# Kernel optimization log

Hardware: AMD Instinct MI355X
Metric: run time of the kernel (lower is better)

The kernel has to match this reference:

```python
import jax, jax.numpy as jnp
import numpy as np

V, L, H, D, DFF = 32000, 6, 8, 64, 1024
DM = H * D  # 512
N, T = 4, 1024
EPS = 1e-3  # keras LayerNormalization default epsilon


def setup_inputs() -> dict:
    key = jax.random.key(0)
    ks = jax.random.split(key, 13)
    s = 0.02
    return {
        "x": jax.random.randint(ks[0], (N, T), 0, V, dtype=jnp.int32),
        "emb": jax.random.normal(ks[1], (V, DM), jnp.float32) * s,
        "Wqkv": jax.random.normal(ks[2], (L, DM, 3 * DM), jnp.float32) * s,
        "bqkv": jnp.zeros((L, 3 * DM), jnp.float32),
        "Wff": jax.random.normal(ks[3], (L, DM, DFF), jnp.float32) * s,
        "bff": jnp.zeros((L, DFF), jnp.float32),
        "Wo": jax.random.normal(ks[4], (L, DFF, DM), jnp.float32) * s,
        "bo": jnp.zeros((L, DM), jnp.float32),
        "g1": jnp.ones((L, DM), jnp.float32),
        "beta1": jnp.zeros((L, DM), jnp.float32),
        "g2": jnp.ones((L, DM), jnp.float32),
        "beta2": jnp.zeros((L, DM), jnp.float32),
    }


def _pos_encoding(seq_len, d_model):
    pos = jnp.arange(seq_len, dtype=jnp.float32)[:, None]
    i = jnp.arange(d_model, dtype=jnp.float32)[None, :]
    angle_rates = 1.0 / jnp.power(10000.0, 2.0 * jnp.floor(i / 2.0) / d_model)
    ang = pos * angle_rates
    even = (jnp.arange(d_model) % 2) == 0
    return jnp.where(even[None, :], jnp.sin(ang), jnp.cos(ang))  # [T, DM]


def _ln(x, g, b):
    m = jnp.mean(x, axis=-1, keepdims=True)
    v = jnp.mean(jnp.square(x - m), axis=-1, keepdims=True)
    return g * (x - m) / jnp.sqrt(v + EPS) + b


def reference(x, emb, Wqkv, bqkv, Wff, bff, Wo, bo, g1, beta1, g2, beta2):
    n, t = x.shape
    h = emb[x] * jnp.sqrt(jnp.float32(DM))          # [N,T,DM]
    h = h + _pos_encoding(t, DM)[None, :, :]
    # causal additive mask: 1 above diagonal, 0 on/below
    mask = 1.0 - jnp.tril(jnp.ones((t, t), jnp.float32))
    neg = mask[None, None, :, :] * -1e9
    scale = 1.0 / jnp.sqrt(jnp.float32(D))
    for l in range(L):
        qkv = h @ Wqkv[l] + bqkv[l]                 # [N,T,3*DM]
        qkv = qkv.reshape(n, t, H, D, 3)
        q, k, v = [jnp.transpose(qkv[..., j], (0, 2, 1, 3)) for j in range(3)]  # [N,H,T,D]
        logits = jnp.einsum("nhtd,nhsd->nhts", q, k) * scale + neg
        w = jax.nn.softmax(logits, axis=-1)
        a = jnp.einsum("nhts,nhsd->nhtd", w, v)     # [N,H,T,D]
        a = jnp.transpose(a, (0, 2, 1, 3)).reshape(n, t, DM)
        h = _ln(h + a, g1[l], beta1[l])
        ff = jax.nn.relu(h @ Wff[l] + bff[l]) @ Wo[l] + bo[l]
        h = _ln(h + ff, g2[l], beta2[l])
    return h
```

## Files before the change

### kernel.cpp

```cpp
#include <hip/hip_runtime.h>
#include <hip/hip_bf16.h>
#include <math.h>

#define DM   512
#define TT   1024
#define NB   4
#define NHD  8
#define LAYERS 6
#define DFFD 1024
#define MROWS (NB*TT)
#define PERBUF (NB*NHD*TT*64)

typedef __bf16 bf16x8 __attribute__((ext_vector_type(8)));
typedef __bf16 bf16x4 __attribute__((ext_vector_type(4)));
typedef float f32x4 __attribute__((ext_vector_type(4)));

__device__ __forceinline__ void gl_lds16(const __bf16* g, __bf16* l) {
    __builtin_amdgcn_global_load_lds((const __attribute__((address_space(1))) void*)g,
                                     (__attribute__((address_space(3))) void*)l, 16, 0, 0);
}

__global__ __launch_bounds__(256) void embed_pos_kernel(const int* __restrict__ x,
    const float* __restrict__ emb, float* __restrict__ h, __bf16* __restrict__ hb)
{
    int row = blockIdx.x;
    int t = row & (TT - 1);
    int tok = x[row];
    const float* e = emb + (size_t)tok * DM;
    float* out = h + (size_t)row * DM;
    __bf16* outb = hb + (size_t)row * DM;
    for (int i = threadIdx.x; i < DM; i += 256) {
        float val = e[i] * 22.62741699796952f;
        int pair = i >> 1;
        float rate = powf(10000.0f, -(float)pair * (1.0f / 256.0f));
        float ang = (float)t * rate;
        float pe = (i & 1) ? cosf(ang) : sinf(ang);
        float v = val + pe;
        out[i] = v;
        outb[i] = (__bf16)v;
    }
}

__global__ __launch_bounds__(256) void convert_all_kernel(
    const float* __restrict__ Wqkv, const float* __restrict__ Wff, const float* __restrict__ Wo,
    __bf16* __restrict__ WtQ, __bf16* __restrict__ WtF, __bf16* __restrict__ WtO)
{
    __shared__ float tile[32][33];
    int l = blockIdx.z;
    int t = blockIdx.x;
    const float* W; __bf16* Wt; int K, N, bx, by;
    if (t < 768)       { W = Wqkv; Wt = WtQ; K = 512;  N = 1536; bx = t & 15;  by = t >> 4; }
    else if (t < 1280) { int u = t - 768;  W = Wff; Wt = WtF; K = 512;  N = 1024; bx = u & 15; by = u >> 4; }
    else               { int u = t - 1280; W = Wo;  Wt = WtO; K = 1024; N = 512;  bx = u & 31; by = u >> 5; }
    int k0 = bx * 32, n0 = by * 32;
    const float* Wl = W + (size_t)l * K * N;
    __bf16* Wtl = Wt + (size_t)l * K * N;
    int tx = threadIdx.x & 31, ty = threadIdx.x >> 5;
    #pragma unroll
    for (int i = ty; i < 32; i += 8)
        tile[i][tx] = Wl[(size_t)(k0 + i) * N + n0 + tx];
    __syncthreads();
    #pragma unroll
    for (int i = ty; i < 32; i += 8)
        Wtl[(size_t)(n0 + i) * K + k0 + tx] = (__bf16)tile[tx][i];
}

__global__ __launch_bounds__(256) void gemm_mfma(const __bf16* __restrict__ A,
    const __bf16* __restrict__ Bt, const float* __restrict__ bias,
    __bf16* __restrict__ Cb, int M, int Nc, int K, int mode)
{
    __shared__ __align__(16) __bf16 As[2][128 * 32];
    __shared__ __align__(16) __bf16 Bs[2][128 * 32];
    int tid = threadIdx.x;
    int lane = tid & 63;
    int wave = tid >> 6;
    int ln = lane & 15, q = lane >> 4;
    int wrow = (wave >> 1) * 64, wcol = (wave & 1) * 64;
    int n0 = blockIdx.x * 128, m0 = blockIdx.y * 128;

    f32x4 acc[4][4] = {};

    const __bf16* Ab = A + (size_t)m0 * K;
    const __bf16* Bb = Bt + (size_t)n0 * K;

    int srow = lane >> 2;
    int scol = (lane & 3) * 8;
    const __bf16* Ag0 = Ab + (size_t)(wave * 32 + srow) * K + scol;
    const __bf16* Ag1 = Ab + (size_t)(wave * 32 + 16 + srow) * K + scol;
    const __bf16* Bg0 = Bb + (size_t)(wave * 32 + srow) * K + scol;
    const __bf16* Bg1 = Bb + (size_t)(wave * 32 + 16 + srow) * K + scol;

    for (int k0 = 0; k0 < K; k0 += 64) {
        __syncthreads();
        #pragma unroll
        for (int p = 0; p < 2; p++) {
            int kp = k0 + p * 32;
            gl_lds16(Ag0 + kp, As[p] + (wave * 32) * 32);
            gl_lds16(Ag1 + kp, As[p] + (wave * 32 + 16) * 32);
            gl_lds16(Bg0 + kp, Bs[p] + (wave * 32) * 32);
            gl_lds16(Bg1 + kp, Bs[p] + (wave * 32 + 16) * 32);
        }
        __syncthreads();

        #pragma unroll
        for (int p = 0; p < 2; p++) {
            bf16x8 af[4], bfr[4];
            #pragma unroll
            for (int mt = 0; mt < 4; mt++)
                af[mt] = *(const bf16x8*)&As[p][(wrow + mt * 16 + ln) * 32 + q * 8];
            #pragma unroll
            for (int nt = 0; nt < 4; nt++)
                bfr[nt] = *(const bf16x8*)&Bs[p][(wcol + nt * 16 + ln) * 32 + q * 8];
            #pragma unroll
            for (int mt = 0; mt < 4; mt++)
                #pragma unroll
                for (int nt = 0; nt < 4; nt++)
                    acc[mt][nt] = __builtin_amdgcn_mfma_f32_16x16x32_bf16(af[mt], bfr[nt], acc[mt][nt], 0, 0, 0);
        }
    }

    #pragma unroll
    for (int mt = 0; mt < 4; mt++) {
        #pragma unroll
        for (int r = 0; r < 4; r++) {
            int m = m0 + wrow + mt * 16 + q * 4 + r;
            #pragma unroll
            for (int nt = 0; nt < 4; nt++) {
                int c = n0 + wcol + nt * 16 + ln;
                float val = acc[mt][nt][r] + bias[c];
                if (mode == 1) {
                    Cb[(size_t)m * Nc + c] = (__bf16)fmaxf(val, 0.f);
                } else {
                    int jj = c % 3;
                    int hd = c / 3;
                    int hh = hd >> 6, d = hd & 63;
                    int n = m >> 10, t = m & (TT - 1);
                    size_t idx;
                    if (jj == 2)
                        idx = 2 * (size_t)PERBUF + (((size_t)(n * NHD + hh) * 64 + d) << 10) + t;
                    else
                        idx = (size_t)jj * PERBUF + (((size_t)(n * NHD + hh) * TT + t) << 6) + d;
                    Cb[idx] = (__bf16)val;
                }
            }
        }
    }
}

__global__ __launch_bounds__(256) void gemm_ff2(const __bf16* __restrict__ A,
    const __bf16* __restrict__ Bt, const float* __restrict__ bias,
    float* __restrict__ C, int M, int Nc, int K)
{
    __shared__ __align__(16) __bf16 As[2][128 * 32];
    __shared__ __align__(16) __bf16 Bs[2][64 * 32];
    int tid = threadIdx.x;
    int lane = tid & 63;
    int wave = tid >> 6;
    int ln = lane & 15, q = lane >> 4;
    int wrow = (wave >> 1) * 64, wcol = (wave & 1) * 32;
    int n0 = blockIdx.x * 64, m0 = blockIdx.y * 128;

    f32x4 acc[4][2] = {};

    const __bf16* Ab = A + (size_t)m0 * K;
    const __bf16* Bb = Bt + (size_t)n0 * K;

    int srow = lane >> 2;
    int scol = (lane & 3) * 8;
    const __bf16* Ag0 = Ab + (size_t)(wave * 32 + srow) * K + scol;
    const __bf16* Ag1 = Ab + (size_t)(wave * 32 + 16 + srow) * K + scol;
    const __bf16* Bg0 = Bb + (size_t)(wave * 16 + srow) * K + scol;

    for (int k0 = 0; k0 < K; k0 += 64) {
        __syncthreads();
        #pragma unroll
        for (int p = 0; p < 2; p++) {
            int kp = k0 + p * 32;
            gl_lds16(Ag0 + kp, As[p] + (wave * 32) * 32);
            gl_lds16(Ag1 + kp, As[p] + (wave * 32 + 16) * 32);
            gl_lds16(Bg0 + kp, Bs[p] + (wave * 16) * 32);
        }
        __syncthreads();

        #pragma unroll
        for (int p = 0; p < 2; p++) {
            bf16x8 af[4], bfr[2];
            #pragma unroll
            for (int mt = 0; mt < 4; mt++)
                af[mt] = *(const bf16x8*)&As[p][(wrow + mt * 16 + ln) * 32 + q * 8];
            #pragma unroll
            for (int nt = 0; nt < 2; nt++)
                bfr[nt] = *(const bf16x8*)&Bs[p][(wcol + nt * 16 + ln) * 32 + q * 8];
            #pragma unroll
            for (int mt = 0; mt < 4; mt++)
                #pragma unroll
                for (int nt = 0; nt < 2; nt++)
                    acc[mt][nt] = __builtin_amdgcn_mfma_f32_16x16x32_bf16(af[mt], bfr[nt], acc[mt][nt], 0, 0, 0);
        }
    }

    #pragma unroll
    for (int mt = 0; mt < 4; mt++) {
        #pragma unroll
        for (int r = 0; r < 4; r++) {
            int m = m0 + wrow + mt * 16 + q * 4 + r;
            #pragma unroll
            for (int nt = 0; nt < 2; nt++) {
                int c = n0 + wcol + nt * 16 + ln;
                C[(size_t)m * Nc + c] = acc[mt][nt][r] + bias[c];
            }
        }
    }
}

#define APAD 72
#define NCHUNK 40
__global__ __launch_bounds__(256) void attn_partial_kernel(const __bf16* __restrict__ qb,
    const __bf16* __restrict__ kb, const __bf16* __restrict__ vtb,
    float* __restrict__ po, float* __restrict__ pden)
{
    __shared__ __bf16 KPs[64 * APAD];
    __shared__ __bf16 Vs[64 * APAD];

    int u = (NCHUNK - 1) - blockIdx.x;
    int nh = blockIdx.y;
    int g, off;
    if (u < 4)       { g = 0; off = 0;  }
    else if (u < 12) { g = 1; off = 4;  }
    else if (u < 24) { g = 2; off = 12; }
    else             { g = 3; off = 24; }
    int rem = u - off;
    int nper = g + 1;
    int qq = rem / nper;
    int c  = rem - qq * nper;
    int qt = g * 4 + qq;
    int st0 = c * 4;
    int st1 = min(st0 + 4, qt + 1);

    int tid = threadIdx.x;
    int lane = tid & 63, w = tid >> 6;
    int ln = lane & 15, q = lane >> 4;

    const __bf16* Kg = kb + (size_t)nh * TT * 64;
    const __bf16* Vg = vtb + (size_t)nh * 64 * TT;

    const __bf16* Qrow = qb + ((size_t)nh * TT + (size_t)qt * 64 + w * 16 + ln) * 64;
    bf16x8 aq0 = *(const bf16x8*)(Qrow + q * 8);
    bf16x8 aq1 = *(const bf16x8*)(Qrow + 32 + q * 8);

    f32x4 o_acc[4] = {};
    float den_reg[4] = {0.f, 0.f, 0.f, 0.f};

    int sr = tid >> 3, scl = (tid & 7) * 8;
    int sr1 = sr + 32;

    for (int st = st0; st < st1; st++) {
        __syncthreads();
        *(bf16x8*)&KPs[sr  * APAD + scl] = *(const bf16x8*)&Kg[(size_t)(st * 64 + sr ) * 64 + scl];
        *(bf16x8*)&Vs [sr  * APAD + scl] = *(const bf16x8*)&Vg[(size_t)sr  * TT + st * 64 + scl];
        *(bf16x8*)&KPs[sr1 * APAD + scl] = *(const bf16x8*)&Kg[(size_t)(st * 64 + sr1) * 64 + scl];
        *(bf16x8*)&Vs [sr1 * APAD + scl] = *(const bf16x8*)&Vg[(size_t)sr1 * TT + st * 64 + scl];
        __syncthreads();

        f32x4 s_acc[4] = {};
        #pragma unroll
        for (int nt = 0; nt < 4; nt++) {
            bf16x8 b0 = *(const bf16x8*)&KPs[(nt * 16 + ln) * APAD + q * 8];
            s_acc[nt] = __builtin_amdgcn_mfma_f32_16x16x32_bf16(aq0, b0, s_acc[nt], 0, 0, 0);
            bf16x8 b1 = *(const bf16x8*)&KPs[(nt * 16 + ln) * APAD + 32 + q * 8];
            s_acc[nt] = __builtin_amdgcn_mfma_f32_16x16x32_bf16(aq1, b1, s_acc[nt], 0, 0, 0);
        }
        __syncthreads();

        bool diag = (st == qt);
        #pragma unroll
        for (int nt = 0; nt < 4; nt++) {
            #pragma unroll
            for (int r = 0; r < 4; r++) {
                int lrow = w * 16 + q * 4 + r;
                int lcol = nt * 16 + ln;
                float p;
                if (diag && lcol > lrow) p = 0.f;
                else p = exp2f(s_acc[nt][r] * 0.18033688011112042f);
                den_reg[r] += p;
                KPs[lrow * APAD + lcol] = (__bf16)p;
            }
        }
        __syncthreads();

        #pragma unroll
        for (int ks = 0; ks < 2; ks++) {
            bf16x8 af = *(const bf16x8*)&Vs[(w * 16 + ln) * APAD + ks * 32 + q * 8];
            #pragma unroll
            for (int nt = 0; nt < 4; nt++) {
                bf16x8 bfr = *(const bf16x8*)&KPs[(nt * 16 + ln) * APAD + ks * 32 + q * 8];
                o_acc[nt] = __builtin_amdgcn_mfma_f32_16x16x32_bf16(af, bfr, o_acc[nt], 0, 0, 0);
            }
        }
    }

    #pragma unroll
    for (int m = 1; m < 16; m <<= 1)
        #pragma unroll
        for (int r = 0; r < 4; r++)
            den_reg[r] += __shfl_xor(den_reg[r], m, 64);
    size_t slot = (size_t)nh * NCHUNK + u;
    if (ln == 0)
        #pragma unroll
        for (int r = 0; r < 4; r++)
            pden[slot * 64 + w * 16 + q * 4 + r] = den_reg[r];

    #pragma unroll
    for (int nt = 0; nt < 4; nt++)
        *(f32x4*)&po[(slot << 12) + (size_t)(nt * 16 + ln) * 64 + w * 16 + q * 4] = o_acc[nt];
}

__global__ __launch_bounds__(256) void add_ln_attn_kernel(float* __restrict__ h,
    __bf16* __restrict__ hb, const float* __restrict__ po, const float* __restrict__ pden,
    const float* __restrict__ g, const float* __restrict__ b)
{
    int w = threadIdx.x >> 6, lane = threadIdx.x & 63;
    int row = (blockIdx.x << 2) + w;
    int n = row >> 10, t = row & (TT - 1);
    int qt = t >> 6, qrow = t & 63;
    int gg = qt >> 2, nc = gg + 1;
    const int offs[4] = {0, 4, 12, 24};
    int u0 = offs[gg] + (qt - gg * 4) * nc;
    int hh = lane >> 3;
    int d0 = (lane & 7) * 8;
    size_t s0 = (size_t)(n * NHD + hh) * NCHUNK + u0;

    f32x4 a0 = {0.f,0.f,0.f,0.f}, a1 = {0.f,0.f,0.f,0.f};
    float den = 0.f;
    for (int c = 0; c < nc; c++) {
        const float* p = po + ((s0 + c) << 12) + (size_t)qrow * 64 + d0;
        a0 += *(const f32x4*)p;
        a1 += *(const f32x4*)(p + 4);
        den += pden[(s0 + c) * 64 + qrow];
    }
    float inv = 1.0f / den;

    size_t base = (size_t)row * DM + lane * 8;
    f32x4 x0 = *(const f32x4*)&h[base];
    f32x4 x1 = *(const f32x4*)&h[base + 4];
    x0 += a0 * inv;
    x1 += a1 * inv;

    float s1 = x0[0]+x0[1]+x0[2]+x0[3] + x1[0]+x1[1]+x1[2]+x1[3];
    float s2 = x0[0]*x0[0]+x0[1]*x0[1]+x0[2]*x0[2]+x0[3]*x0[3]
             + x1[0]*x1[0]+x1[1]*x1[1]+x1[2]*x1[2]+x1[3]*x1[3];
    #pragma unroll
    for (int m = 1; m < 64; m <<= 1) {
        s1 += __shfl_xor(s1, m, 64);
        s2 += __shfl_xor(s2, m, 64);
    }
    float mean = s1 * (1.0f / 512.0f);
    float var = s2 * (1.0f / 512.0f) - mean * mean;
    float rstd = rsqrtf(var + 1e-3f);

    f32x4 gg0 = *(const f32x4*)&g[lane * 8];
    f32x4 gg1 = *(const f32x4*)&g[lane * 8 + 4];
    f32x4 bb0 = *(const f32x4*)&b[lane * 8];
    f32x4 bb1 = *(const f32x4*)&b[lane * 8 + 4];
    f32x4 o0, o1;
    bf16x8 pb;
    #pragma unroll
    for (int i = 0; i < 4; i++) {
        o0[i] = gg0[i] * ((x0[i] - mean) * rstd) + bb0[i];
        o1[i] = gg1[i] * ((x1[i] - mean) * rstd) + bb1[i];
        pb[i] = (__bf16)o0[i];
        pb[4 + i] = (__bf16)o1[i];
    }
    *(f32x4*)&h[base] = o0;
    *(f32x4*)&h[base + 4] = o1;
    *(bf16x8*)(hb + base) = pb;
}

__global__ __launch_bounds__(256) void add_ln_kernel(float* __restrict__ h,
    __bf16* __restrict__ hb, const float* __restrict__ a,
    const float* __restrict__ g, const float* __restrict__ b)
{
    int w = threadIdx.x >> 6, lane = threadIdx.x & 63;
    int row = (blockIdx.x << 2) + w;
    size_t base4 = (size_t)row * (DM / 4);
    const float4* h4 = (const float4*)h;
    const float4* a4 = (const float4*)a;
    float4 x0 = h4[base4 + lane];
    float4 x1 = h4[base4 + 64 + lane];
    float4 y0 = a4[base4 + lane];
    float4 y1 = a4[base4 + 64 + lane];
    x0.x += y0.x; x0.y += y0.y; x0.z += y0.z; x0.w += y0.w;
    x1.x += y1.x; x1.y += y1.y; x1.z += y1.z; x1.w += y1.w;
    float s1 = x0.x + x0.y + x0.z + x0.w + x1.x + x1.y + x1.z + x1.w;
    float s2 = x0.x*x0.x + x0.y*x0.y + x0.z*x0.z + x0.w*x0.w
             + x1.x*x1.x + x1.y*x1.y + x1.z*x1.z + x1.w*x1.w;
    #pragma unroll
    for (int m = 1; m < 64; m <<= 1) {
        s1 += __shfl_xor(s1, m, 64);
        s2 += __shfl_xor(s2, m, 64);
    }
    float mean = s1 * (1.0f / 512.0f);
    float var = s2 * (1.0f / 512.0f) - mean * mean;
    float rstd = rsqrtf(var + 1e-3f);
    const float4* g4 = (const float4*)g;
    const float4* b4 = (const float4*)b;
    float4 gg0 = g4[lane], gg1 = g4[64 + lane];
    float4 bb0 = b4[lane], bb1 = b4[64 + lane];
    float4 o0, o1;
    o0.x = gg0.x * ((x0.x - mean) * rstd) + bb0.x;
    o0.y = gg0.y * ((x0.y - mean) * rstd) + bb0.y;
    o0.z = gg0.z * ((x0.z - mean) * rstd) + bb0.z;
    o0.w = gg0.w * ((x0.w - mean) * rstd) + bb0.w;
    o1.x = gg1.x * ((x1.x - mean) * rstd) + bb1.x;
    o1.y = gg1.y * ((x1.y - mean) * rstd) + bb1.y;
    o1.z = gg1.z * ((x1.z - mean) * rstd) + bb1.z;
    o1.w = gg1.w * ((x1.w - mean) * rstd) + bb1.w;
    ((float4*)h)[base4 + lane] = o0;
    ((float4*)h)[base4 + 64 + lane] = o1;
    bf16x4 p0, p1;
    p0[0] = (__bf16)o0.x; p0[1] = (__bf16)o0.y; p0[2] = (__bf16)o0.z; p0[3] = (__bf16)o0.w;
    p1[0] = (__bf16)o1.x; p1[1] = (__bf16)o1.y; p1[2] = (__bf16)o1.z; p1[3] = (__bf16)o1.w;
    *(bf16x4*)(hb + (size_t)row * DM + lane * 4) = p0;
    *(bf16x4*)(hb + (size_t)row * DM + 256 + lane * 4) = p1;
}

extern "C" void kernel_launch(void* const* d_in, const int* in_sizes, int n_in,
                              void* d_out, int out_size, void* d_ws, size_t ws_size,
                              hipStream_t stream) {
    const int*   x     = (const int*)d_in[0];
    const float* emb   = (const float*)d_in[1];
    const float* Wqkv  = (const float*)d_in[2];
    const float* bqkv  = (const float*)d_in[3];
    const float* Wff   = (const float*)d_in[4];
    const float* bff   = (const float*)d_in[5];
    const float* Wo    = (const float*)d_in[6];
    const float* bo    = (const float*)d_in[7];
    const float* g1    = (const float*)d_in[8];
    const float* beta1 = (const float*)d_in[9];
    const float* g2    = (const float*)d_in[10];
    const float* beta2 = (const float*)d_in[11];

    float* h = (float*)d_out;
    char* w = (char*)d_ws;
    __bf16* qkvb = (__bf16*)w;
    __bf16* ffb  = (__bf16*)w;
    float*  abuf = (float*)(w + 25165824);
    __bf16* hb   = (__bf16*)(w + 33554432);
    __bf16* WtQ  = (__bf16*)(w + 37748736);
    __bf16* WtF  = (__bf16*)(w + 47185920);
    __bf16* WtO  = (__bf16*)(w + 53477376);
    float*  po   = (float*)(w + 59768832);
    float*  pden = (float*)(w + 80740352);

    convert_all_kernel<<<dim3(1792, 1, LAYERS), 256, 0, stream>>>(
        Wqkv, Wff, Wo, WtQ, WtF, WtO);

    embed_pos_kernel<<<MROWS, 256, 0, stream>>>(x, emb, h, hb);

    for (int l = 0; l < LAYERS; l++) {
        const float* bqkv_l = bqkv + (size_t)l * (3 * DM);
        const float* bff_l  = bff  + (size_t)l * DFFD;
        const float* bo_l   = bo   + (size_t)l * DM;

        gemm_mfma<<<dim3(12, 32), 256, 0, stream>>>(
            hb, WtQ + (size_t)l * 1536 * 512, bqkv_l, qkvb, MROWS, 3 * DM, DM, 2);

        attn_partial_kernel<<<dim3(NCHUNK, NB * NHD), 256, 0, stream>>>(
            qkvb, qkvb + PERBUF, qkvb + 2 * (size_t)PERBUF, po, pden);

        add_ln_attn_kernel<<<MROWS / 4, 256, 0, stream>>>(
            h, hb, po, pden, g1 + l * DM, beta1 + l * DM);

        gemm_mfma<<<dim3(8, 32), 256, 0, stream>>>(
            hb, WtF + (size_t)l * 1024 * 512, bff_l, ffb, MROWS, DFFD, DM, 1);

        gemm_ff2<<<dim3(8, 32), 256, 0, stream>>>(
            ffb, WtO + (size_t)l * 512 * 1024, bo_l, abuf, MROWS, DM, DFFD);

        add_ln_kernel<<<MROWS / 4, 256, 0, stream>>>(h, hb, abuf, g2 + l * DM, beta2 + l * DM);
    }
}
```

Before: 736.7 us.

## Permute QKV weight columns for vectorized epilogue; async swizzled K/V loads in attention

The QKV weight rows and bias are reordered at conversion time so each GEMM output tile maps to a single Q, K or V buffer. This removes the per-element mod/div in the epilogue and lets the V^T store use 4-wide bf16 writes. The attention kernel now loads K and V with global_load_lds into XOR-swizzled shared buffers, with V double-buffered and the next tile prefetched during the PV matmul, and P gets its own buffer. This drops one barrier per tile and overlaps loads with compute. The cost is extra LDS and tighter ordering between the K reuse and the prefetch.

```diff
diff --git a/kernel.cpp b/kernel.cpp
--- a/kernel.cpp
+++ b/kernel.cpp
@@ -43,13 +43,15 @@
 
 __global__ __launch_bounds__(256) void convert_all_kernel(
     const float* __restrict__ Wqkv, const float* __restrict__ Wff, const float* __restrict__ Wo,
-    __bf16* __restrict__ WtQ, __bf16* __restrict__ WtF, __bf16* __restrict__ WtO)
+    const float* __restrict__ bqkv,
+    __bf16* __restrict__ WtQ, __bf16* __restrict__ WtF, __bf16* __restrict__ WtO,
+    float* __restrict__ bqkv_p)
 {
     __shared__ float tile[32][33];
     int l = blockIdx.z;
     int t = blockIdx.x;
-    const float* W; __bf16* Wt; int K, N, bx, by;
-    if (t < 768)       { W = Wqkv; Wt = WtQ; K = 512;  N = 1536; bx = t & 15;  by = t >> 4; }
+    const float* W; __bf16* Wt; int K, N, bx, by; bool perm = false;
+    if (t < 768)       { W = Wqkv; Wt = WtQ; K = 512;  N = 1536; bx = t & 15;  by = t >> 4; perm = true; }
     else if (t < 1280) { int u = t - 768;  W = Wff; Wt = WtF; K = 512;  N = 1024; bx = u & 15; by = u >> 4; }
     else               { int u = t - 1280; W = Wo;  Wt = WtO; K = 1024; N = 512;  bx = u & 31; by = u >> 5; }
     int k0 = bx * 32, n0 = by * 32;
@@ -59,10 +61,17 @@
     #pragma unroll
     for (int i = ty; i < 32; i += 8)
         tile[i][tx] = Wl[(size_t)(k0 + i) * N + n0 + tx];
+    if (perm && bx == 0 && ty == 0) {
+        int c = n0 + tx;
+        bqkv_p[l * 1536 + (c % 3) * 512 + c / 3] = bqkv[(size_t)l * 1536 + c];
+    }
     __syncthreads();
     #pragma unroll
-    for (int i = ty; i < 32; i += 8)
-        Wtl[(size_t)(n0 + i) * K + k0 + tx] = (__bf16)tile[tx][i];
+    for (int i = ty; i < 32; i += 8) {
+        int c = n0 + i;
+        int row = perm ? ((c % 3) * 512 + c / 3) : c;
+        Wtl[(size_t)row * K + k0 + tx] = (__bf16)tile[tx][i];
+    }
 }
 
 __global__ __launch_bounds__(256) void gemm_mfma(const __bf16* __restrict__ A,
@@ -121,26 +130,38 @@
 
     #pragma unroll
     for (int mt = 0; mt < 4; mt++) {
-        #pragma unroll
-        for (int r = 0; r < 4; r++) {
-            int m = m0 + wrow + mt * 16 + q * 4 + r;
+        int mbase = m0 + wrow + mt * 16 + q * 4;
+        if (mode == 1) {
+            #pragma unroll
+            for (int r = 0; r < 4; r++) {
+                int m = mbase + r;
+                #pragma unroll
+                for (int nt = 0; nt < 4; nt++) {
+                    int c = n0 + wcol + nt * 16 + ln;
+                    float val = acc[mt][nt][r] + bias[c];
+                    Cb[(size_t)m * Nc + c] = (__bf16)fmaxf(val, 0.f);
+                }
+            }
+        } else {
+            int n = mbase >> 10, t = mbase & (TT - 1);
             #pragma unroll
             for (int nt = 0; nt < 4; nt++) {
                 int c = n0 + wcol + nt * 16 + ln;
-                float val = acc[mt][nt][r] + bias[c];
-                if (mode == 1) {
-                    Cb[(size_t)m * Nc + c] = (__bf16)fmaxf(val, 0.f);
+                int buf = c >> 9;
+                int hd = c & 511;
+                int hh = hd >> 6, d = hd & 63;
+                float bv = bias[c];
+                if (buf == 2) {
+                    size_t idx = 2 * (size_t)PERBUF + (((size_t)(n * NHD + hh) * 64 + d) << 10) + t;
+                    bf16x4 v4;
+                    #pragma unroll
+                    for (int r = 0; r < 4; r++) v4[r] = (__bf16)(acc[mt][nt][r] + bv);
+                    *(bf16x4*)&Cb[idx] = v4;
                 } else {
-                    int jj = c % 3;
-                    int hd = c / 3;
-                    int hh = hd >> 6, d = hd & 63;
-                    int n = m >> 10, t = m & (TT - 1);
-                    size_t idx;
-                    if (jj == 2)
-                        idx = 2 * (size_t)PERBUF + (((size_t)(n * NHD + hh) * 64 + d) << 10) + t;
-                    else
-                        idx = (size_t)jj * PERBUF + (((size_t)(n * NHD + hh) * TT + t) << 6) + d;
-                    Cb[idx] = (__bf16)val;
+                    size_t base = (size_t)buf * PERBUF + (((size_t)(n * NHD + hh) * TT + t) << 6) + d;
+                    #pragma unroll
+                    for (int r = 0; r < 4; r++)
+                        Cb[base + (size_t)(r << 6)] = (__bf16)(acc[mt][nt][r] + bv);
                 }
             }
         }
@@ -213,14 +234,15 @@
     }
 }
 
-#define APAD 72
+#define PPAD 72
 #define NCHUNK 40
 __global__ __launch_bounds__(256) void attn_partial_kernel(const __bf16* __restrict__ qb,
     const __bf16* __restrict__ kb, const __bf16* __restrict__ vtb,
     float* __restrict__ po, float* __restrict__ pden)
 {
-    __shared__ __bf16 KPs[64 * APAD];
-    __shared__ __bf16 Vs[64 * APAD];
+    __shared__ __align__(16) __bf16 Ksh[64 * 64];
+    __shared__ __align__(16) __bf16 Vsh[2][64 * 64];
+    __shared__ __align__(16) __bf16 Ps[64 * PPAD];
 
     int u = (NCHUNK - 1) - blockIdx.x;
     int nh = blockIdx.y;
@@ -248,29 +270,39 @@
     bf16x8 aq0 = *(const bf16x8*)(Qrow + q * 8);
     bf16x8 aq1 = *(const bf16x8*)(Qrow + 32 + q * 8);
 
+    int srow = lane >> 3;
+    int swz  = ((lane & 7) ^ srow) << 3;
+    int r0 = (w * 2 + 0) * 8 + srow;
+    int r1 = (w * 2 + 1) * 8 + srow;
+    const __bf16* Kg0 = Kg + (size_t)r0 * 64 + swz;
+    const __bf16* Kg1 = Kg + (size_t)r1 * 64 + swz;
+    const __bf16* Vg0 = Vg + (size_t)r0 * TT + swz;
+    const __bf16* Vg1 = Vg + (size_t)r1 * TT + swz;
+    __bf16* Kd0 = Ksh + (w * 2 + 0) * 512;
+    __bf16* Kd1 = Ksh + (w * 2 + 1) * 512;
+
     f32x4 o_acc[4] = {};
     float den_reg[4] = {0.f, 0.f, 0.f, 0.f};
 
-    int sr = tid >> 3, scl = (tid & 7) * 8;
-    int sr1 = sr + 32;
-
+    int cur = 0;
+    gl_lds16(Kg0 + st0 * 4096, Kd0);
+    gl_lds16(Kg1 + st0 * 4096, Kd1);
+    gl_lds16(Vg0 + st0 * 64, Vsh[0] + (w * 2 + 0) * 512);
+    gl_lds16(Vg1 + st0 * 64, Vsh[0] + (w * 2 + 1) * 512);
+
+    int kswz = ln & 7;
     for (int st = st0; st < st1; st++) {
         __syncthreads();
-        *(bf16x8*)&KPs[sr  * APAD + scl] = *(const bf16x8*)&Kg[(size_t)(st * 64 + sr ) * 64 + scl];
-        *(bf16x8*)&Vs [sr  * APAD + scl] = *(const bf16x8*)&Vg[(size_t)sr  * TT + st * 64 + scl];
-        *(bf16x8*)&KPs[sr1 * APAD + scl] = *(const bf16x8*)&Kg[(size_t)(st * 64 + sr1) * 64 + scl];
-        *(bf16x8*)&Vs [sr1 * APAD + scl] = *(const bf16x8*)&Vg[(size_t)sr1 * TT + st * 64 + scl];
-        __syncthreads();
 
         f32x4 s_acc[4] = {};
         #pragma unroll
         for (int nt = 0; nt < 4; nt++) {
-            bf16x8 b0 = *(const bf16x8*)&KPs[(nt * 16 + ln) * APAD + q * 8];
+            int r = nt * 16 + ln;
+            bf16x8 b0 = *(const bf16x8*)&Ksh[r * 64 + ((q ^ kswz) << 3)];
             s_acc[nt] = __builtin_amdgcn_mfma_f32_16x16x32_bf16(aq0, b0, s_acc[nt], 0, 0, 0);
-            bf16x8 b1 = *(const bf16x8*)&KPs[(nt * 16 + ln) * APAD + 32 + q * 8];
+            bf16x8 b1 = *(const bf16x8*)&Ksh[r * 64 + (((q + 4) ^ kswz) << 3)];
             s_acc[nt] = __builtin_amdgcn_mfma_f32_16x16x32_bf16(aq1, b1, s_acc[nt], 0, 0, 0);
         }
-        __syncthreads();
 
         bool diag = (st == qt);
         #pragma unroll
@@ -283,20 +315,28 @@
                 if (diag && lcol > lrow) p = 0.f;
                 else p = exp2f(s_acc[nt][r] * 0.18033688011112042f);
                 den_reg[r] += p;
-                KPs[lrow * APAD + lcol] = (__bf16)p;
+                Ps[lrow * PPAD + lcol] = (__bf16)p;
             }
         }
         __syncthreads();
 
+        if (st + 1 < st1) {
+            gl_lds16(Kg0 + (st + 1) * 4096, Kd0);
+            gl_lds16(Kg1 + (st + 1) * 4096, Kd1);
+            gl_lds16(Vg0 + (st + 1) * 64, Vsh[cur ^ 1] + (w * 2 + 0) * 512);
+            gl_lds16(Vg1 + (st + 1) * 64, Vsh[cur ^ 1] + (w * 2 + 1) * 512);
+        }
+
         #pragma unroll
         for (int ks = 0; ks < 2; ks++) {
-            bf16x8 af = *(const bf16x8*)&Vs[(w * 16 + ln) * APAD + ks * 32 + q * 8];
+            bf16x8 af = *(const bf16x8*)&Vsh[cur][(w * 16 + ln) * 64 + (((ks * 4 + q) ^ kswz) << 3)];
             #pragma unroll
             for (int nt = 0; nt < 4; nt++) {
-                bf16x8 bfr = *(const bf16x8*)&KPs[(nt * 16 + ln) * APAD + ks * 32 + q * 8];
+                bf16x8 bfr = *(const bf16x8*)&Ps[(nt * 16 + ln) * PPAD + ks * 32 + q * 8];
                 o_acc[nt] = __builtin_amdgcn_mfma_f32_16x16x32_bf16(af, bfr, o_acc[nt], 0, 0, 0);
             }
         }
+        cur ^= 1;
     }
 
     #pragma unroll
@@ -451,19 +491,19 @@
     __bf16* WtO  = (__bf16*)(w + 53477376);
     float*  po   = (float*)(w + 59768832);
     float*  pden = (float*)(w + 80740352);
+    float*  bqkv_p = (float*)(w + 81068032);
 
     convert_all_kernel<<<dim3(1792, 1, LAYERS), 256, 0, stream>>>(
-        Wqkv, Wff, Wo, WtQ, WtF, WtO);
+        Wqkv, Wff, Wo, bqkv, WtQ, WtF, WtO, bqkv_p);
 
     embed_pos_kernel<<<MROWS, 256, 0, stream>>>(x, emb, h, hb);
 
     for (int l = 0; l < LAYERS; l++) {
-        const float* bqkv_l = bqkv + (size_t)l * (3 * DM);
         const float* bff_l  = bff  + (size_t)l * DFFD;
         const float* bo_l   = bo   + (size_t)l * DM;
 
         gemm_mfma<<<dim3(12, 32), 256, 0, stream>>>(
-            hb, WtQ + (size_t)l * 1536 * 512, bqkv_l, qkvb, MROWS, 3 * DM, DM, 2);
+            hb, WtQ + (size_t)l * 1536 * 512, bqkv_p + l * 1536, qkvb, MROWS, 3 * DM, DM, 2);
 
         attn_partial_kernel<<<dim3(NCHUNK, NB * NHD), 256, 0, stream>>>(
             qkvb, qkvb + PERBUF, qkvb + 2 * (size_t)PERBUF, po, pden);
```

Result: faster. 672.9 us (-8.7%).
